# Kernel tuning notes

Hardware: AMD Instinct MI355X
Metric: run time of the kernel (lower is better)

Reference implementation:

```python
import jax, jax.numpy as jnp
import numpy as np

B, OBS, LAT, NXT, E, HG, H = 8192, 128, 32, 128, 8, 256, 256


def setup_inputs() -> dict:
    key = jax.random.key(0)
    ks = jax.random.split(key, 20)
    d_in = OBS + LAT

    def w(k, shape, fan_in):
        return jax.random.uniform(k, shape, jnp.float32, -1.0, 1.0) * (np.sqrt(3.0) / np.sqrt(fan_in)).astype(np.float32)

    inp = {
        "x": jax.random.normal(ks[0], (B, OBS), jnp.float32),
        "z": jax.random.normal(ks[1], (B, LAT), jnp.float32),
        # gating MLP: (obs+lat) -> hg -> hg -> hg -> E
        "gw0": w(ks[2], (d_in, HG), d_in), "gb0": jnp.zeros((HG,), jnp.float32),
        "gw1": w(ks[3], (HG, HG), HG),    "gb1": jnp.zeros((HG,), jnp.float32),
        "gw2": w(ks[4], (HG, HG), HG),    "gb2": jnp.zeros((HG,), jnp.float32),
        "gw3": w(ks[5], (HG, E), HG),     "gb3": jnp.zeros((E,), jnp.float32),
        # expert weight stacks (kaiming-uniform-style init, bias = 0.01)
        "w0": w(ks[6], (E, d_in, H), d_in * H),      "b0": jnp.full((E, H), 0.01, jnp.float32),
        "w1": w(ks[7], (E, H + LAT, H), (H + LAT) * H), "b1": jnp.full((E, H), 0.01, jnp.float32),
        "w2": w(ks[8], (E, H + LAT, NXT), (H + LAT) * NXT), "b2": jnp.full((E, NXT), 0.01, jnp.float32),
    }
    return inp


def reference(x, z, gw0, gb0, gw1, gb1, gw2, gb2, gw3, gb3, w0, b0, w1, b1, w2, b2):
    xz = jnp.concatenate((x, z), axis=1)  # [B, obs+lat]
    # gating MLP (ELU activations, linear head) -> softmax coefficients over experts
    g = jax.nn.elu(xz @ gw0 + gb0)
    g = jax.nn.elu(g @ gw1 + gb1)
    g = jax.nn.elu(g @ gw2 + gb2)
    coef = jax.nn.softmax(g @ gw3 + gb3, axis=1)  # [B, E]

    layer_out = x
    for w, b, act in ((w0, b0, jax.nn.elu), (w1, b1, jax.nn.elu), (w2, b2, None)):
        inp = jnp.concatenate((layer_out, z), axis=1)  # [B, i]
        # coefficient-weighted expert mixing fused with the per-sample matvec:
        # equals (coef @ flat_weight).view(B,i,o) consumed by baddbmm in the original
        out = jnp.einsum('bi,eio,be->bo', inp, w, coef) + coef @ b
        layer_out = act(out) if act is not None else out
    return layer_out
```

## Files before the change

### kernel.cpp

```cpp
#include <hip/hip_runtime.h>
#include <hip/hip_bf16.h>

typedef _Float16 half_t;
typedef __attribute__((ext_vector_type(8))) _Float16 half8;
typedef __attribute__((ext_vector_type(4))) _Float16 half4;
typedef __attribute__((ext_vector_type(4))) float float4v;

#define BSZ 8192
#define NT 1024
#define ACTSTR 280
#define XSTR 152
#define ZSTR 40

#define RING_SLOT 1024
#define RING_WAVE (3 * RING_SLOT)
#define OFF_SX   (16 * RING_WAVE)
#define OFF_SB0  (OFF_SX + 32 * XSTR)
#define OFF_SB1  (OFF_SB0 + 32 * ACTSTR)
#define OFF_SZ   (OFF_SB1 + 32 * ACTSTR)
#define HALFS_TOTAL (OFF_SZ + 32 * ZSTR)
#define OFF_BIAS_B (HALFS_TOTAL * 2)
#define OFF_LOG_B  (OFF_BIAS_B + 8192)
#define OFF_CF_B   (OFF_LOG_B + 1024)
#define SMEM_BYTES (OFF_CF_B + 1024)

__device__ __forceinline__ float elu_fast(float v) {
    return v > 0.f ? v : (__expf(v) - 1.f);
}

template <int N>
__device__ __forceinline__ void wait_vm() {
    if constexpr (N == 0)      asm volatile("s_waitcnt vmcnt(0)" ::: "memory");
    else if constexpr (N == 1) asm volatile("s_waitcnt vmcnt(1)" ::: "memory");
    else if constexpr (N == 2) asm volatile("s_waitcnt vmcnt(2)" ::: "memory");
    else                       asm volatile("s_waitcnt vmcnt(4)" ::: "memory");
}

__device__ __forceinline__ void lds_dma16(half_t* lds, const half_t* g) {
    __builtin_amdgcn_global_load_lds(
        (const __attribute__((address_space(1))) void*)g,
        (__attribute__((address_space(3))) void*)lds, 16, 0, 0);
}

template <int EXPP, int NPASS, int CH, int MT, bool ZLAST, int ACT, int DST>
__device__ __forceinline__ void layer_run(
    half_t* sm, const half_t* sSrc, int sstr,
    const half_t* __restrict__ W, int NS,
    const float* __restrict__ bias, int biasN, const float* sCf, float* sBias,
    half_t* sDst, float* __restrict__ gOut, int ldg,
    int row0, int strip, int mrow, int wv, int lane, int l15, int quad) {
    constexpr int TOT = NPASS * CH;
    const size_t estr = (size_t)NS * CH * 512;
    const int col = strip * 16 + l15;
    half_t* ring = sm + wv * RING_WAVE;
    const half_t* sZ = sm + OFF_SZ;
    float* myBias = sBias + wv * 128;

    if (quad == 0) {
#pragma unroll
        for (int e = 0; e < NPASS * EXPP; ++e)
            myBias[e * 16 + l15] = bias[e * biasN + col];
    }
    wait_vm<0>();

    float4v acc[EXPP][MT];
    float part[MT][4];

    const half_t* wp = W + (size_t)strip * CH * 512 + lane * 8;
    int s_i = 0, c_i = 0;
    auto issue = [&]() {
        half_t* slot = ring + s_i * RING_SLOT;
#pragma unroll
        for (int e = 0; e < EXPP; ++e) lds_dma16(slot + e * 512, wp + (size_t)e * estr);
        s_i = (s_i == 2) ? 0 : s_i + 1;
        wp += 512;
        if (++c_i == CH) { c_i = 0; wp += EXPP * estr - CH * 512; }
    };

    const half_t* aBase = sSrc + (mrow + l15) * sstr + quad * 8;
    const half_t* zBase = sZ + (mrow + l15) * ZSTR + quad * 8;
    int s_c = 0, c_c = 0, h_c = 0;
    auto body = [&]() {
        half8 a[MT];
#pragma unroll
        for (int mt = 0; mt < MT; ++mt)
            a[mt] = (ZLAST && c_c == CH - 1)
                        ? *(const half8*)&zBase[mt * 16 * ZSTR]
                        : *(const half8*)&aBase[mt * 16 * sstr + c_c * 32];
        if (c_c == 0) {
#pragma unroll
            for (int e = 0; e < EXPP; ++e)
#pragma unroll
                for (int mt = 0; mt < MT; ++mt) acc[e][mt] = (float4v){0.f, 0.f, 0.f, 0.f};
        }
        const half_t* slot = ring + s_c * RING_SLOT + lane * 8;
#pragma unroll
        for (int e = 0; e < EXPP; ++e) {
            half8 b = *(const half8*)&slot[e * 512];
#pragma unroll
            for (int mt = 0; mt < MT; ++mt)
                acc[e][mt] = __builtin_amdgcn_mfma_f32_16x16x32_f16(a[mt], b, acc[e][mt], 0, 0, 0);
        }
        if (c_c == CH - 1) {
            const int eoff = h_c * EXPP;
#pragma unroll
            for (int mt = 0; mt < MT; ++mt)
#pragma unroll
                for (int r = 0; r < 4; ++r) {
                    const int rl = mrow + mt * 16 + quad * 4 + r;
                    float val = 0.f;
#pragma unroll
                    for (int e = 0; e < EXPP; ++e) {
                        const float ab = acc[e][mt][r] + myBias[(eoff + e) * 16 + l15];
                        val += (EXPP * NPASS == 1) ? ab : sCf[rl * 8 + eoff + e] * ab;
                    }
                    part[mt][r] = (h_c == 0) ? val : part[mt][r] + val;
                    if (h_c == NPASS - 1) {
                        float o = part[mt][r];
                        if (DST == 0) {
                            if (ACT) o = elu_fast(o);
                            sDst[rl * ACTSTR + col] = (half_t)o;
                        } else {
                            gOut[(size_t)(row0 + rl) * ldg + col] = o;
                        }
                    }
                }
        }
        s_c = (s_c == 2) ? 0 : s_c + 1;
        if (++c_c == CH) { c_c = 0; ++h_c; }
    };

    issue();
    issue();
#pragma unroll 1
    for (int it = 0; it < TOT - 2; ++it) {
        issue();
        wait_vm<2 * EXPP>();
        body();
    }
    wait_vm<EXPP>();
    body();
    wait_vm<0>();
    body();
}

__device__ __forceinline__ void layer_logits(
    const half_t* sSrc, const half_t* __restrict__ W,
    const float* __restrict__ bias, float* sLog, int wv, int lane, int l15, int quad) {
    if (wv != 0) return;
    float4v acc[2] = {(float4v){0.f, 0.f, 0.f, 0.f}, (float4v){0.f, 0.f, 0.f, 0.f}};
#pragma unroll
    for (int c = 0; c < 8; ++c) {
        half8 a0 = *(const half8*)&sSrc[l15 * ACTSTR + c * 32 + quad * 8];
        half8 a1 = *(const half8*)&sSrc[(16 + l15) * ACTSTR + c * 32 + quad * 8];
        half8 b = *(const half8*)&W[c * 512 + lane * 8];
        acc[0] = __builtin_amdgcn_mfma_f32_16x16x32_f16(a0, b, acc[0], 0, 0, 0);
        acc[1] = __builtin_amdgcn_mfma_f32_16x16x32_f16(a1, b, acc[1], 0, 0, 0);
    }
    if (l15 < 8) {
        const float bvv = bias[l15];
#pragma unroll
        for (int mt = 0; mt < 2; ++mt)
#pragma unroll
            for (int r = 0; r < 4; ++r)
                sLog[(mt * 16 + quad * 4 + r) * 8 + l15] = acc[mt][r] + bvv;
    }
}

__global__ __launch_bounds__(NT) void fused_mann(
    const float* __restrict__ x, const float* __restrict__ z,
    const half_t* __restrict__ Wg0, const half_t* __restrict__ Wg1,
    const half_t* __restrict__ Wg2, const half_t* __restrict__ Wg3,
    const float* __restrict__ gb0, const float* __restrict__ gb1,
    const float* __restrict__ gb2, const float* __restrict__ gb3,
    const half_t* __restrict__ W0, const half_t* __restrict__ W1,
    const half_t* __restrict__ W2, const float* __restrict__ b0,
    const float* __restrict__ b1, const float* __restrict__ b2,
    float* __restrict__ out) {
    extern __shared__ __align__(16) char dynsm[];
    half_t* sm = (half_t*)dynsm;
    half_t* sX = sm + OFF_SX;
    half_t* sB0 = sm + OFF_SB0;
    half_t* sB1 = sm + OFF_SB1;
    half_t* sZ = sm + OFF_SZ;
    float* sBias = (float*)(dynsm + OFF_BIAS_B);
    float* sLog = (float*)(dynsm + OFF_LOG_B);
    float* sCf = (float*)(dynsm + OFF_CF_B);

    const int tid = threadIdx.x;
    const int row0 = blockIdx.x * 32;
    const int lane = tid & 63, wv = tid >> 6;
    const int l15 = lane & 15, quad = lane >> 4;

    for (int i = tid; i < 32 * 128; i += NT) {
        int r = i >> 7, c = i & 127;
        sX[r * XSTR + c] = (half_t)x[(size_t)(row0 + r) * 128 + c];
    }
    for (int i = tid; i < 32 * 32; i += NT) {
        int r = i >> 5, c = i & 31;
        sZ[r * ZSTR + c] = (half_t)z[(size_t)(row0 + r) * 32 + c];
    }
    __syncthreads();

    layer_run<1, 1, 5, 2, true, 1, 0>(sm, sX, XSTR, Wg0, 16, gb0, 256, nullptr, sBias,
                                      sB0, nullptr, 0, row0, wv, 0, wv, lane, l15, quad);
    __syncthreads();
    layer_run<1, 1, 8, 2, false, 1, 0>(sm, sB0, ACTSTR, Wg1, 16, gb1, 256, nullptr, sBias,
                                       sB1, nullptr, 0, row0, wv, 0, wv, lane, l15, quad);
    __syncthreads();
    layer_run<1, 1, 8, 2, false, 1, 0>(sm, sB1, ACTSTR, Wg2, 16, gb2, 256, nullptr, sBias,
                                       sB0, nullptr, 0, row0, wv, 0, wv, lane, l15, quad);
    __syncthreads();
    layer_logits(sB0, Wg3, gb3, sLog, wv, lane, l15, quad);
    __syncthreads();
    if (tid < 32) {
        float v[8], m = -1e30f;
#pragma unroll
        for (int e = 0; e < 8; ++e) { v[e] = sLog[tid * 8 + e]; m = fmaxf(m, v[e]); }
        float sum = 0.f;
#pragma unroll
        for (int e = 0; e < 8; ++e) { v[e] = __expf(v[e] - m); sum += v[e]; }
        float inv = 1.f / sum;
#pragma unroll
        for (int e = 0; e < 8; ++e) sCf[tid * 8 + e] = v[e] * inv;
    }
    __syncthreads();
    layer_run<2, 4, 5, 2, true, 1, 0>(sm, sX, XSTR, W0, 16, b0, 256, sCf, sBias,
                                      sB1, nullptr, 0, row0, wv, 0, wv, lane, l15, quad);
    __syncthreads();
    layer_run<2, 4, 9, 2, true, 1, 0>(sm, sB1, ACTSTR, W1, 16, b1, 256, sCf, sBias,
                                      sB0, nullptr, 0, row0, wv, 0, wv, lane, l15, quad);
    __syncthreads();
    layer_run<2, 4, 9, 1, true, 0, 2>(sm, sB0, ACTSTR, W2, 8, b2, 128, sCf, sBias,
                                      nullptr, out, 128, row0, wv & 7, (wv >> 3) * 16,
                                      wv, lane, l15, quad);
}

struct WDesc { const float* src; half_t* dst; int K, N, Npad, blk0; };
struct WPack { WDesc d[7]; };

__global__ __launch_bounds__(256) void conv_w_all(WPack pk) {
    __shared__ float t[32][33];
    const int bid = blockIdx.x;
    int di = 0;
#pragma unroll
    for (int i = 1; i < 7; ++i)
        if (bid >= pk.d[i].blk0) di = i;
    const WDesc d = pk.d[di];
    const int NS = d.Npad >> 4, CHN = d.K >> 5;
    const int ntiles = d.Npad / 32, ktiles = CHN;
    int local = bid - d.blk0;
    const int e = local / (ktiles * ntiles);
    local %= ktiles * ntiles;
    const int k0 = (local / ntiles) * 32, n0 = (local % ntiles) * 32;
    const int tr = threadIdx.x >> 3;
    const int tc = (threadIdx.x & 7) * 4;

    float4 v = {0.f, 0.f, 0.f, 0.f};
    if (n0 + tc < d.N)
        v = *(const float4*)&d.src[((size_t)e * d.K + k0 + tr) * d.N + n0 + tc];
    t[tr][tc] = v.x; t[tr][tc + 1] = v.y; t[tr][tc + 2] = v.z; t[tr][tc + 3] = v.w;
    __syncthreads();
    half4 h;
#pragma unroll
    for (int i = 0; i < 4; ++i) h[i] = (half_t)t[tc + i][tr];
    const int n = n0 + tr;
    const size_t blk = ((size_t)e * NS + (n >> 4)) * CHN + (k0 >> 5);
    const int off = ((tc >> 3) * 16 + (n & 15)) * 8 + (tc & 7);
    *(half4*)&d.dst[blk * 512 + off] = h;
}

extern "C" void kernel_launch(void* const* d_in, const int* in_sizes, int n_in,
                              void* d_out, int out_size, void* d_ws, size_t ws_size,
                              hipStream_t stream) {
    const float* x   = (const float*)d_in[0];
    const float* z   = (const float*)d_in[1];
    const float* gw0 = (const float*)d_in[2];
    const float* gb0 = (const float*)d_in[3];
    const float* gw1 = (const float*)d_in[4];
    const float* gb1 = (const float*)d_in[5];
    const float* gw2 = (const float*)d_in[6];
    const float* gb2 = (const float*)d_in[7];
    const float* gw3 = (const float*)d_in[8];
    const float* gb3 = (const float*)d_in[9];
    const float* w0  = (const float*)d_in[10];
    const float* b0  = (const float*)d_in[11];
    const float* w1  = (const float*)d_in[12];
    const float* b1  = (const float*)d_in[13];
    const float* w2  = (const float*)d_in[14];
    const float* b2  = (const float*)d_in[15];

    char* p = (char*)d_ws;
    auto take = [&](size_t bytes) { char* r = p; p += bytes; return r; };
    half_t* Wg0 = (half_t*)take((size_t)256 * 160 * 2);
    half_t* Wg1 = (half_t*)take((size_t)256 * 256 * 2);
    half_t* Wg2 = (half_t*)take((size_t)256 * 256 * 2);
    half_t* Wg3 = (half_t*)take((size_t)32 * 256 * 2);
    half_t* W0  = (half_t*)take((size_t)8 * 256 * 160 * 2);
    half_t* W1  = (half_t*)take((size_t)8 * 256 * 288 * 2);
    half_t* W2  = (half_t*)take((size_t)8 * 128 * 288 * 2);
    float* out  = (float*)d_out;

    WPack pk;
    int blk = 0;
    auto mk = [&](int i, const float* s, half_t* dst, int K, int N, int Npad, int E) {
        pk.d[i] = WDesc{s, dst, K, N, Npad, blk};
        blk += E * (K / 32) * (Npad / 32);
    };
    mk(0, gw0, Wg0, 160, 256, 256, 1);
    mk(1, gw1, Wg1, 256, 256, 256, 1);
    mk(2, gw2, Wg2, 256, 256, 256, 1);
    mk(3, gw3, Wg3, 256, 8, 32, 1);
    mk(4, w0, W0, 160, 256, 256, 8);
    mk(5, w1, W1, 288, 256, 256, 8);
    mk(6, w2, W2, 288, 128, 128, 8);

    hipFuncSetAttribute((const void*)fused_mann,
                        hipFuncAttributeMaxDynamicSharedMemorySize, SMEM_BYTES);

    conv_w_all<<<dim3(blk), dim3(256), 0, stream>>>(pk);
    fused_mann<<<dim3(BSZ / 32), dim3(NT), SMEM_BYTES, stream>>>(
        x, z, Wg0, Wg1, Wg2, Wg3, gb0, gb1, gb2, gb3,
        W0, W1, W2, b0, b1, b2, out);
}
```

Before: 140.0 us.

## Replace LDS DMA ring pipeline with direct register weight loads in fully unrolled loops

Drops the per-wave three-slot LDS ring filled by global_load_lds DMA and its manual vmcnt waits. Each layer now loads weight fragments straight from global memory into registers inside fully unrolled pass and chunk loops, and reads bias values into registers instead of staging them in LDS. This removes LDS write and read traffic for weights and cuts shared memory use, which could allow more occupancy. In exchange, latency hiding now depends on the compiler scheduling the unrolled global loads, and register pressure goes up.

```diff
diff --git a/kernel.cpp b/kernel.cpp
--- a/kernel.cpp
+++ b/kernel.cpp
@@ -5,6 +5,7 @@
 typedef __attribute__((ext_vector_type(8))) _Float16 half8;
 typedef __attribute__((ext_vector_type(4))) _Float16 half4;
 typedef __attribute__((ext_vector_type(4))) float float4v;
+typedef __attribute__((ext_vector_type(2))) float float2v;
 
 #define BSZ 8192
 #define NT 1024
@@ -12,136 +13,90 @@
 #define XSTR 152
 #define ZSTR 40
 
-#define RING_SLOT 1024
-#define RING_WAVE (3 * RING_SLOT)
-#define OFF_SX   (16 * RING_WAVE)
-#define OFF_SB0  (OFF_SX + 32 * XSTR)
-#define OFF_SB1  (OFF_SB0 + 32 * ACTSTR)
-#define OFF_SZ   (OFF_SB1 + 32 * ACTSTR)
+#define OFF_SX 0
+#define OFF_SB0 (OFF_SX + 32 * XSTR)
+#define OFF_SB1 (OFF_SB0 + 32 * ACTSTR)
+#define OFF_SZ (OFF_SB1 + 32 * ACTSTR)
 #define HALFS_TOTAL (OFF_SZ + 32 * ZSTR)
-#define OFF_BIAS_B (HALFS_TOTAL * 2)
-#define OFF_LOG_B  (OFF_BIAS_B + 8192)
-#define OFF_CF_B   (OFF_LOG_B + 1024)
+#define OFF_LOG_B (HALFS_TOTAL * 2)
+#define OFF_CF_B (OFF_LOG_B + 1024)
 #define SMEM_BYTES (OFF_CF_B + 1024)
 
 __device__ __forceinline__ float elu_fast(float v) {
     return v > 0.f ? v : (__expf(v) - 1.f);
 }
 
-template <int N>
-__device__ __forceinline__ void wait_vm() {
-    if constexpr (N == 0)      asm volatile("s_waitcnt vmcnt(0)" ::: "memory");
-    else if constexpr (N == 1) asm volatile("s_waitcnt vmcnt(1)" ::: "memory");
-    else if constexpr (N == 2) asm volatile("s_waitcnt vmcnt(2)" ::: "memory");
-    else                       asm volatile("s_waitcnt vmcnt(4)" ::: "memory");
-}
-
-__device__ __forceinline__ void lds_dma16(half_t* lds, const half_t* g) {
-    __builtin_amdgcn_global_load_lds(
-        (const __attribute__((address_space(1))) void*)g,
-        (__attribute__((address_space(3))) void*)lds, 16, 0, 0);
-}
-
 template <int EXPP, int NPASS, int CH, int MT, bool ZLAST, int ACT, int DST>
 __device__ __forceinline__ void layer_run(
-    half_t* sm, const half_t* sSrc, int sstr,
+    const half_t* sSrc, int sstr, const half_t* sZ,
     const half_t* __restrict__ W, int NS,
-    const float* __restrict__ bias, int biasN, const float* sCf, float* sBias,
+    const float* __restrict__ bias, int biasN, const float* sCf,
     half_t* sDst, float* __restrict__ gOut, int ldg,
-    int row0, int strip, int mrow, int wv, int lane, int l15, int quad) {
-    constexpr int TOT = NPASS * CH;
+    int row0, int strip, int mrow, int lane, int l15, int quad) {
     const size_t estr = (size_t)NS * CH * 512;
     const int col = strip * 16 + l15;
-    half_t* ring = sm + wv * RING_WAVE;
-    const half_t* sZ = sm + OFF_SZ;
-    float* myBias = sBias + wv * 128;
-
-    if (quad == 0) {
-#pragma unroll
-        for (int e = 0; e < NPASS * EXPP; ++e)
-            myBias[e * 16 + l15] = bias[e * biasN + col];
-    }
-    wait_vm<0>();
-
-    float4v acc[EXPP][MT];
-    float part[MT][4];
-
-    const half_t* wp = W + (size_t)strip * CH * 512 + lane * 8;
-    int s_i = 0, c_i = 0;
-    auto issue = [&]() {
-        half_t* slot = ring + s_i * RING_SLOT;
-#pragma unroll
-        for (int e = 0; e < EXPP; ++e) lds_dma16(slot + e * 512, wp + (size_t)e * estr);
-        s_i = (s_i == 2) ? 0 : s_i + 1;
-        wp += 512;
-        if (++c_i == CH) { c_i = 0; wp += EXPP * estr - CH * 512; }
-    };
-
+    const half_t* wbase = W + (size_t)strip * CH * 512 + lane * 8;
     const half_t* aBase = sSrc + (mrow + l15) * sstr + quad * 8;
     const half_t* zBase = sZ + (mrow + l15) * ZSTR + quad * 8;
-    int s_c = 0, c_c = 0, h_c = 0;
-    auto body = [&]() {
-        half8 a[MT];
+
+    float part[MT][4];
+#pragma unroll
+    for (int h = 0; h < NPASS; ++h) {
+        float bv[EXPP];
+#pragma unroll
+        for (int e = 0; e < EXPP; ++e)
+            bv[e] = bias[(size_t)(h * EXPP + e) * biasN + col];
+
+        float4v acc[EXPP][MT];
+#pragma unroll
+        for (int e = 0; e < EXPP; ++e)
+#pragma unroll
+            for (int mt = 0; mt < MT; ++mt) acc[e][mt] = (float4v){0.f, 0.f, 0.f, 0.f};
+
+#pragma unroll
+        for (int c = 0; c < CH; ++c) {
+            half8 a[MT];
+#pragma unroll
+            for (int mt = 0; mt < MT; ++mt)
+                a[mt] = (ZLAST && c == CH - 1)
+                            ? *(const half8*)&zBase[mt * 16 * ZSTR]
+                            : *(const half8*)&aBase[mt * 16 * sstr + c * 32];
+            half8 b[EXPP];
+#pragma unroll
+            for (int e = 0; e < EXPP; ++e)
+                b[e] = *(const half8*)&wbase[(size_t)(h * EXPP + e) * estr + c * 512];
+#pragma unroll
+            for (int e = 0; e < EXPP; ++e)
+#pragma unroll
+                for (int mt = 0; mt < MT; ++mt)
+                    acc[e][mt] = __builtin_amdgcn_mfma_f32_16x16x32_f16(a[mt], b[e], acc[e][mt], 0, 0, 0);
+        }
+
 #pragma unroll
         for (int mt = 0; mt < MT; ++mt)
-            a[mt] = (ZLAST && c_c == CH - 1)
-                        ? *(const half8*)&zBase[mt * 16 * ZSTR]
-                        : *(const half8*)&aBase[mt * 16 * sstr + c_c * 32];
-        if (c_c == 0) {
-#pragma unroll
-            for (int e = 0; e < EXPP; ++e)
-#pragma unroll
-                for (int mt = 0; mt < MT; ++mt) acc[e][mt] = (float4v){0.f, 0.f, 0.f, 0.f};
-        }
-        const half_t* slot = ring + s_c * RING_SLOT + lane * 8;
-#pragma unroll
-        for (int e = 0; e < EXPP; ++e) {
-            half8 b = *(const half8*)&slot[e * 512];
-#pragma unroll
-            for (int mt = 0; mt < MT; ++mt)
-                acc[e][mt] = __builtin_amdgcn_mfma_f32_16x16x32_f16(a[mt], b, acc[e][mt], 0, 0, 0);
-        }
-        if (c_c == CH - 1) {
-            const int eoff = h_c * EXPP;
-#pragma unroll
-            for (int mt = 0; mt < MT; ++mt)
-#pragma unroll
-                for (int r = 0; r < 4; ++r) {
-                    const int rl = mrow + mt * 16 + quad * 4 + r;
-                    float val = 0.f;
-#pragma unroll
-                    for (int e = 0; e < EXPP; ++e) {
-                        const float ab = acc[e][mt][r] + myBias[(eoff + e) * 16 + l15];
-                        val += (EXPP * NPASS == 1) ? ab : sCf[rl * 8 + eoff + e] * ab;
-                    }
-                    part[mt][r] = (h_c == 0) ? val : part[mt][r] + val;
-                    if (h_c == NPASS - 1) {
-                        float o = part[mt][r];
-                        if (DST == 0) {
-                            if (ACT) o = elu_fast(o);
-                            sDst[rl * ACTSTR + col] = (half_t)o;
-                        } else {
-                            gOut[(size_t)(row0 + rl) * ldg + col] = o;
-                        }
+#pragma unroll
+            for (int r = 0; r < 4; ++r) {
+                const int rl = mrow + mt * 16 + quad * 4 + r;
+                float val;
+                if constexpr (EXPP * NPASS == 1) {
+                    val = acc[0][mt][r] + bv[0];
+                } else {
+                    const float2v cf = *(const float2v*)&sCf[rl * 8 + h * EXPP];
+                    val = cf[0] * (acc[0][mt][r] + bv[0]);
+                    val += cf[1] * (acc[1][mt][r] + bv[1]);
+                }
+                part[mt][r] = (h == 0) ? val : part[mt][r] + val;
+                if (h == NPASS - 1) {
+                    float o = part[mt][r];
+                    if (DST == 0) {
+                        if (ACT) o = elu_fast(o);
+                        sDst[rl * ACTSTR + col] = (half_t)o;
+                    } else {
+                        gOut[(size_t)(row0 + rl) * ldg + col] = o;
                     }
                 }
-        }
-        s_c = (s_c == 2) ? 0 : s_c + 1;
-        if (++c_c == CH) { c_c = 0; ++h_c; }
-    };
-
-    issue();
-    issue();
-#pragma unroll 1
-    for (int it = 0; it < TOT - 2; ++it) {
-        issue();
-        wait_vm<2 * EXPP>();
-        body();
-    }
-    wait_vm<EXPP>();
-    body();
-    wait_vm<0>();
-    body();
+            }
+    }
 }
 
 __device__ __forceinline__ void layer_logits(
@@ -183,7 +138,6 @@
     half_t* sB0 = sm + OFF_SB0;
     half_t* sB1 = sm + OFF_SB1;
     half_t* sZ = sm + OFF_SZ;
-    float* sBias = (float*)(dynsm + OFF_BIAS_B);
     float* sLog = (float*)(dynsm + OFF_LOG_B);
     float* sCf = (float*)(dynsm + OFF_CF_B);
 
@@ -202,14 +156,14 @@
     }
     __syncthreads();
 
-    layer_run<1, 1, 5, 2, true, 1, 0>(sm, sX, XSTR, Wg0, 16, gb0, 256, nullptr, sBias,
-                                      sB0, nullptr, 0, row0, wv, 0, wv, lane, l15, quad);
-    __syncthreads();
-    layer_run<1, 1, 8, 2, false, 1, 0>(sm, sB0, ACTSTR, Wg1, 16, gb1, 256, nullptr, sBias,
-                                       sB1, nullptr, 0, row0, wv, 0, wv, lane, l15, quad);
-    __syncthreads();
-    layer_run<1, 1, 8, 2, false, 1, 0>(sm, sB1, ACTSTR, Wg2, 16, gb2, 256, nullptr, sBias,
-                                       sB0, nullptr, 0, row0, wv, 0, wv, lane, l15, quad);
+    layer_run<1, 1, 5, 2, true, 1, 0>(sX, XSTR, sZ, Wg0, 16, gb0, 256, nullptr,
+                                      sB0, nullptr, 0, row0, wv, 0, lane, l15, quad);
+    __syncthreads();
+    layer_run<1, 1, 8, 2, false, 1, 0>(sB0, ACTSTR, sZ, Wg1, 16, gb1, 256, nullptr,
+                                       sB1, nullptr, 0, row0, wv, 0, lane, l15, quad);
+    __syncthreads();
+    layer_run<1, 1, 8, 2, false, 1, 0>(sB1, ACTSTR, sZ, Wg2, 16, gb2, 256, nullptr,
+                                       sB0, nullptr, 0, row0, wv, 0, lane, l15, quad);
     __syncthreads();
     layer_logits(sB0, Wg3, gb3, sLog, wv, lane, l15, quad);
     __syncthreads();
@@ -225,15 +179,15 @@
         for (int e = 0; e < 8; ++e) sCf[tid * 8 + e] = v[e] * inv;
     }
     __syncthreads();
-    layer_run<2, 4, 5, 2, true, 1, 0>(sm, sX, XSTR, W0, 16, b0, 256, sCf, sBias,
-                                      sB1, nullptr, 0, row0, wv, 0, wv, lane, l15, quad);
-    __syncthreads();
-    layer_run<2, 4, 9, 2, true, 1, 0>(sm, sB1, ACTSTR, W1, 16, b1, 256, sCf, sBias,
-                                      sB0, nullptr, 0, row0, wv, 0, wv, lane, l15, quad);
-    __syncthreads();
-    layer_run<2, 4, 9, 1, true, 0, 2>(sm, sB0, ACTSTR, W2, 8, b2, 128, sCf, sBias,
+    layer_run<2, 4, 5, 2, true, 1, 0>(sX, XSTR, sZ, W0, 16, b0, 256, sCf,
+                                      sB1, nullptr, 0, row0, wv, 0, lane, l15, quad);
+    __syncthreads();
+    layer_run<2, 4, 9, 2, true, 1, 0>(sB1, ACTSTR, sZ, W1, 16, b1, 256, sCf,
+                                      sB0, nullptr, 0, row0, wv, 0, lane, l15, quad);
+    __syncthreads();
+    layer_run<2, 4, 9, 1, true, 0, 2>(sB0, ACTSTR, sZ, W2, 8, b2, 128, sCf,
                                       nullptr, out, 128, row0, wv & 7, (wv >> 3) * 16,
-                                      wv, lane, l15, quad);
+                                      lane, l15, quad);
 }
 
 struct WDesc { const float* src; half_t* dst; int K, N, Npad, blk0; };
```

New measurement: 146.3 us. 1.05x slower.
